# Kernel tuning notes

Measured on AMD Instinct MI355X. Metric: run time of the kernel, lower is better.

The kernel has to match this reference:

```python
import jax, jax.numpy as jnp
import numpy as np

ANGSTROM_TO_METER = 1e-10
COULOMB_CONSTANT = 8987551792.3
ELECTRON_CHARGE = 1.602176634e-19
EV_TO_JOULE = 1.602176634e-19
COUL_DAMPING_BETA = 18.7
R0_METER = 2.2 * ANGSTROM_TO_METER
EWALD_P = 0.3275911
EWALD_A = (0.254829592, -0.284496736, 1.421413741, -1.453152027, 1.061405429)
EWALD_F = 2.0

N_ATOMS = 200000
N_EDGES = 8000000
N_GRAPHS = 256


def setup_inputs() -> dict:
    key = jax.random.key(0)
    k1, k2, k3, k4, k5 = jax.random.split(key, 5)
    dij = jax.random.normal(k1, (N_EDGES, 3), dtype=jnp.float32)  # Angstrom
    pred_charge = jax.random.normal(k2, (N_ATOMS,), dtype=jnp.float32)  # e
    g_ewald = jnp.full((1,), 3.0e9, dtype=jnp.float32)  # 1/m (~0.3 1/A)
    row = jax.random.randint(k3, (N_EDGES,), 0, N_ATOMS)
    col = jax.random.randint(k4, (N_EDGES,), 0, N_ATOMS)
    batch = jnp.sort(jax.random.randint(k5, (N_ATOMS,), 0, N_GRAPHS))
    return {"dij": dij, "pred_charge": pred_charge, "g_ewald": g_ewald,
            "row": row, "col": col, "batch": batch}


def reference(dij, pred_charge, g_ewald, row, col, batch):
    n_atoms = pred_charge.shape[0]
    dij_m = dij * ANGSTROM_TO_METER                      # [E,3] meters
    rij = jnp.sqrt(jnp.sum(dij_m * dij_m, axis=-1))      # [E]
    q = pred_charge * ELECTRON_CHARGE                    # Coulombs
    prefactor = COULOMB_CONSTANT * q[row] * q[col] / rij
    # exponential short-range damping below r0
    damp = jnp.where(rij < R0_METER,
                     jnp.exp(-COUL_DAMPING_BETA * (R0_METER - rij) / R0_METER),
                     jnp.ones_like(rij))
    ecoul = 0.5 * prefactor * damp
    fcoul = prefactor * damp / rij
    # Ewald real-space correction via Abramowitz-Stegun erfc polynomial
    grij = g_ewald[0] * rij
    expm2 = jnp.exp(-grij * grij)
    t = 1.0 / (1.0 + EWALD_P * grij)
    a0, a1, a2, a3, a4 = EWALD_A
    erfc = t * (a0 + t * (a1 + t * (a2 + t * (a3 + t * a4)))) * expm2
    ecoul = ecoul + prefactor * (erfc - 1.0)
    fcoul = fcoul + prefactor * (erfc + EWALD_F * grij * expm2 - 1.0) / rij
    # per-edge force vector, converted J/m -> eV/A
    fij = dij_m * (fcoul / rij)[:, None]                 # [E,3]
    fij_ev = fij * ANGSTROM_TO_METER / EV_TO_JOULE
    ecoul_ev = ecoul / EV_TO_JOULE
    # scatter edge->atom (by row), then atom->molecule (by batch)
    e_atom = jax.ops.segment_sum(ecoul_ev, row, num_segments=n_atoms)
    coul_energy = jax.ops.segment_sum(e_atom, batch, num_segments=N_GRAPHS)
    force_row = jax.ops.segment_sum(fij_ev, row, num_segments=n_atoms)
    force_col = jax.ops.segment_sum(fij_ev, col, num_segments=n_atoms)
    coul_force = force_row - force_col
    return coul_energy, coul_force
```

## Files before the change

kernel.cpp:

```cpp
#include <hip/hip_runtime.h>
#include <hip/hip_fp16.h>

#define N_GRAPHS_C 256
#define CHUNK_LOG 12
#define CHUNK (1 << CHUNK_LOG)
#define MAXB 64
#define NSLICE 12
#define NSLICE_FB 10
#define TPA 256
#define TPBB 512
#define SD 64
#define FP_SCALE 1024.0f
#define FP_INV   (1.0f / 1024.0f)

__device__ __forceinline__ void edge_math(
    float dx, float dy, float dz, float qr, float qc, float gA,
    float& fx, float& fy, float& fz, float& ecoul)
{
    const float KEV = (float)(8987551792.3 * 1.602176634e-9);
    float r2 = dx * dx + dy * dy + dz * dz;
    float inv_r = rsqrtf(r2);
    float rA = r2 * inv_r;

    float pref = KEV * qr * qc * inv_r;

    float damp = 1.0f;
    if (rA < 2.2f)
        damp = __expf(-18.7f * (2.2f - rA) * (1.0f / 2.2f));

    float grij = gA * rA;
    float expm2 = __expf(-grij * grij);
    float t = 1.0f / (1.0f + 0.3275911f * grij);
    float erfc = t * (0.254829592f +
                 t * (-0.284496736f +
                 t * (1.421413741f +
                 t * (-1.453152027f +
                 t * 1.061405429f)))) * expm2;

    ecoul = pref * (0.5f * damp + (erfc - 1.0f));
    float S = damp + erfc + 2.0f * grij * expm2 - 1.0f;
    float fs = pref * S * (inv_r * inv_r);
    fx = dx * fs; fy = dy * fs; fz = dz * fs;
}

__device__ __forceinline__ uint2 pack_rec(float fx, float fy, float fz, unsigned lid)
{
    uint2 u;
    u.x = __builtin_bit_cast(unsigned, __floats2half2_rn(fx, fy));
    u.y = (__builtin_bit_cast(unsigned, __floats2half2_rn(fz, 0.0f)) & 0xFFFFu) |
          (lid << 16);
    return u;
}

__device__ __forceinline__ void acc_rec(int* acc, unsigned w0, unsigned w1)
{
    float2 xy = __half22float2(__builtin_bit_cast(__half2, w0));
    float fz = __half2float(__builtin_bit_cast(__half2, w1).x);
    unsigned idx = w1 >> 16;
    atomicAdd(&acc[idx],             __float2int_rn(xy.x * FP_SCALE));
    atomicAdd(&acc[CHUNK + idx],     __float2int_rn(xy.y * FP_SCALE));
    atomicAdd(&acc[2 * CHUNK + idx], __float2int_rn(fz   * FP_SCALE));
}

__global__ __launch_bounds__(256) void prep_qg(
    const float* __restrict__ q, const int* __restrict__ batch,
    float2* __restrict__ qg, float* __restrict__ ovf, int n_atoms)
{
    int i = blockIdx.x * 256 + threadIdx.x;
    if (i < n_atoms) {
        qg[i] = make_float2(q[i], __int_as_float(batch[i]));
        ovf[3 * i + 0] = 0.f;
        ovf[3 * i + 1] = 0.f;
        ovf[3 * i + 2] = 0.f;
    }
}

__global__ __launch_bounds__(TPA) void passA(
    const float* __restrict__ dij, const float2* __restrict__ qg,
    const float* __restrict__ g_ewald,
    const int* __restrict__ row, const int* __restrict__ col,
    uint2* __restrict__ records, int cap,
    unsigned* __restrict__ cnt_table,
    float* __restrict__ e_part,
    float* __restrict__ ovf,
    int n_edges, int nb, int tile_g)
{
    __shared__ uint2    stage[MAXB][SD];
    __shared__ unsigned scnt[MAXB];
    __shared__ unsigned cnt[MAXB];
    __shared__ float    e_graph[4 * N_GRAPHS_C];

    int tid  = threadIdx.x;
    int wid  = tid >> 6;
    int lane = tid & 63;
    if (tid < MAXB) { scnt[tid] = 0u; cnt[tid] = 0u; }
    for (int i = tid; i < 4 * N_GRAPHS_C; i += TPA) e_graph[i] = 0.f;
    __syncthreads();

    float* e_my = &e_graph[wid * N_GRAPHS_C];

    int n4 = n_edges >> 2;
    int gbase = blockIdx.x * tile_g;
    int g1 = min(gbase + tile_g, n4);
    int nph = tile_g / TPA;

    const int4* row4 = (const int4*)row;
    const int4* col4 = (const int4*)col;
    const float4* dij4 = (const float4*)dij;

    const float gA = g_ewald[0] * 1e-10f;
    size_t blk_base = (size_t)blockIdx.x * nb * cap;

    int4 r_cur = make_int4(0, 0, 0, 0), c_cur = make_int4(0, 0, 0, 0);
    float2 vr_cur[4], vc_cur[4];
    {
        int g = gbase + tid;
        if (g < g1) { r_cur = row4[g]; c_cur = col4[g]; }
        vr_cur[0] = qg[r_cur.x]; vc_cur[0] = qg[c_cur.x];
        vr_cur[1] = qg[r_cur.y]; vc_cur[1] = qg[c_cur.y];
        vr_cur[2] = qg[r_cur.z]; vc_cur[2] = qg[c_cur.z];
        vr_cur[3] = qg[r_cur.w]; vc_cur[3] = qg[c_cur.w];
    }

    for (int p = 0; p < nph; ++p) {
        int g = gbase + p * TPA + tid;

        int4 r_nxt = make_int4(0, 0, 0, 0), c_nxt = make_int4(0, 0, 0, 0);
        if (p + 1 < nph && g + TPA < g1) {
            r_nxt = row4[g + TPA]; c_nxt = col4[g + TPA];
        }

        if (g < g1) {
            float4 d0 = dij4[3 * g + 0];
            float4 d1 = dij4[3 * g + 1];
            float4 d2 = dij4[3 * g + 2];
            float ex[4] = {d0.x, d0.w, d1.z, d2.y};
            float ey[4] = {d0.y, d1.x, d1.w, d2.z};
            float ez[4] = {d0.z, d1.y, d2.x, d2.w};
            int rr[4] = {r_cur.x, r_cur.y, r_cur.z, r_cur.w};
            int cc[4] = {c_cur.x, c_cur.y, c_cur.z, c_cur.w};

            #pragma unroll
            for (int j = 0; j < 4; ++j) {
                int r = rr[j], c = cc[j];
                float fx, fy, fz, ec;
                edge_math(ex[j], ey[j], ez[j], vr_cur[j].x, vc_cur[j].x, gA,
                          fx, fy, fz, ec);

                atomicAdd(&e_my[__float_as_int(vr_cur[j].y)], ec);

                int br = r >> CHUNK_LOG, bc = c >> CHUNK_LOG;
                unsigned pr = atomicAdd(&scnt[br], 1u);
                unsigned pc = atomicAdd(&scnt[bc], 1u);
                if (pr < SD)
                    stage[br][pr] = pack_rec(fx, fy, fz, (unsigned)(r & (CHUNK - 1)));
                else {
                    atomicAdd(&ovf[3 * r + 0], fx);
                    atomicAdd(&ovf[3 * r + 1], fy);
                    atomicAdd(&ovf[3 * r + 2], fz);
                }
                if (pc < SD)
                    stage[bc][pc] = pack_rec(-fx, -fy, -fz, (unsigned)(c & (CHUNK - 1)));
                else {
                    atomicAdd(&ovf[3 * c + 0], -fx);
                    atomicAdd(&ovf[3 * c + 1], -fy);
                    atomicAdd(&ovf[3 * c + 2], -fz);
                }
            }
        }

        float2 vr_n[4], vc_n[4];
        vr_n[0] = qg[r_nxt.x]; vc_n[0] = qg[c_nxt.x];
        vr_n[1] = qg[r_nxt.y]; vc_n[1] = qg[c_nxt.y];
        vr_n[2] = qg[r_nxt.z]; vc_n[2] = qg[c_nxt.z];
        vr_n[3] = qg[r_nxt.w]; vc_n[3] = qg[c_nxt.w];

        __syncthreads();

        for (int b = wid; b < nb; b += TPA / 64) {
            unsigned m = min(scnt[b], (unsigned)SD);
            unsigned base = 0;
            if (lane == 0) base = atomicAdd(&cnt[b], m);
            base = (unsigned)__shfl((int)base, 0, 64);
            for (unsigned i = lane; i < m; i += 64) {
                uint2 rv = stage[b][i];
                unsigned slot = base + i;
                if (slot < (unsigned)cap) {
                    records[blk_base + (size_t)b * cap + slot] = rv;
                } else {
                    float2 xy = __half22float2(__builtin_bit_cast(__half2, rv.x));
                    float fzv = __half2float(__builtin_bit_cast(__half2, rv.y).x);
                    int atom = (b << CHUNK_LOG) + (int)(rv.y >> 16);
                    atomicAdd(&ovf[3 * atom + 0], xy.x);
                    atomicAdd(&ovf[3 * atom + 1], xy.y);
                    atomicAdd(&ovf[3 * atom + 2], fzv);
                }
            }
            if (lane == 0) scnt[b] = 0u;
        }
        __syncthreads();

        r_cur = r_nxt; c_cur = c_nxt;
        #pragma unroll
        for (int j = 0; j < 4; ++j) { vr_cur[j] = vr_n[j]; vc_cur[j] = vc_n[j]; }
    }

    if (tid < nb) cnt_table[(size_t)blockIdx.x * nb + tid] = min(cnt[tid], (unsigned)cap);
    for (int g2 = tid; g2 < N_GRAPHS_C; g2 += TPA)
        e_part[(size_t)blockIdx.x * N_GRAPHS_C + g2] =
            e_graph[g2] + e_graph[N_GRAPHS_C + g2] +
            e_graph[2 * N_GRAPHS_C + g2] + e_graph[3 * N_GRAPHS_C + g2];
}

__global__ __launch_bounds__(TPBB) void passB(
    const uint2* __restrict__ records, int cap,
    const unsigned* __restrict__ cnt_table,
    int* __restrict__ partial, int nblkA, int nb, int nslice)
{
    __shared__ int acc[3 * CHUNK];

    int b = blockIdx.x / nslice;
    int s = blockIdx.x % nslice;
    int k0 = (int)((long long)s * nblkA / nslice);
    int k1 = (int)((long long)(s + 1) * nblkA / nslice);

    for (int i = threadIdx.x; i < 3 * CHUNK; i += TPBB) acc[i] = 0;
    __syncthreads();

    int wid  = threadIdx.x >> 6;
    int lane = threadIdx.x & 63;

    for (int k = k0 + wid; k < k1; k += TPBB / 64) {
        unsigned n = cnt_table[(size_t)k * nb + b];
        const uint2* rec = records + ((size_t)k * nb + b) * cap;
        const uint4* rec4 = (const uint4*)rec;
        unsigned nh = n >> 1;
        for (unsigned i = lane; i < nh; i += 64) {
            uint4 v = rec4[i];
            acc_rec(acc, v.x, v.y);
            acc_rec(acc, v.z, v.w);
        }
        if ((n & 1u) && lane == 0) {
            uint2 t = rec[n - 1];
            acc_rec(acc, t.x, t.y);
        }
    }
    __syncthreads();

    int* dst = partial + (size_t)blockIdx.x * 3 * CHUNK;
    for (int i = threadIdx.x; i < 3 * CHUNK; i += TPBB) dst[i] = acc[i];
}

__global__ __launch_bounds__(256) void fin_force(
    const int* __restrict__ partial, const float* __restrict__ ovf,
    const float* __restrict__ e_part,
    float* __restrict__ force, float* __restrict__ energy,
    int n_atoms, int nslice, int nblkA, int nfblk)
{
    if ((int)blockIdx.x >= nfblk) {
        int g = (blockIdx.x - nfblk) * 4 + (threadIdx.x >> 6);
        int lane = threadIdx.x & 63;
        float s = 0.f;
        for (int k = lane; k < nblkA; k += 64)
            s += e_part[(size_t)k * N_GRAPHS_C + g];
        for (int off = 32; off > 0; off >>= 1) s += __shfl_down(s, off, 64);
        if (lane == 0) energy[g] = s;
        return;
    }
    int a = blockIdx.x * 256 + threadIdx.x;
    if (a >= n_atoms) return;
    int b = a >> CHUNK_LOG, l = a & (CHUNK - 1);
    long long sx = 0, sy = 0, sz = 0;
    const int* p = partial + (size_t)b * nslice * 3 * CHUNK + l;
    for (int s = 0; s < nslice; ++s) {
        const int* ps = p + (size_t)s * 3 * CHUNK;
        sx += ps[0]; sy += ps[CHUNK]; sz += ps[2 * CHUNK];
    }
    force[3 * a + 0] = ovf[3 * a + 0] + (float)sx * FP_INV;
    force[3 * a + 1] = ovf[3 * a + 1] + (float)sy * FP_INV;
    force[3 * a + 2] = ovf[3 * a + 2] + (float)sz * FP_INV;
}

__global__ __launch_bounds__(1024) void chunk_kernel(
    const float* __restrict__ dij, const float* __restrict__ q,
    const float* __restrict__ g_ewald,
    const int* __restrict__ row, const int* __restrict__ col,
    float* __restrict__ partial, int n_edges, int n_chunks, int n_slices)
{
    __shared__ float acc[CHUNK * 4];
    int c = blockIdx.x % n_chunks;
    int p = blockIdx.x / n_chunks;
    int cbase = c << CHUNK_LOG;
    for (int i = threadIdx.x; i < CHUNK * 4; i += 1024) acc[i] = 0.f;
    __syncthreads();
    const float gA = g_ewald[0] * 1e-10f;
    int n4 = (n_edges + 3) >> 2;
    int g0 = (int)((long long)p * n4 / n_slices);
    int g1 = (int)((long long)(p + 1) * n4 / n_slices);
    const int4* row4 = (const int4*)row;
    const int4* col4 = (const int4*)col;
    for (int g = g0 + threadIdx.x; g < g1; g += 1024) {
        int4 r4 = row4[g];
        int4 c4 = col4[g];
        int rr[4] = {r4.x, r4.y, r4.z, r4.w};
        int cc[4] = {c4.x, c4.y, c4.z, c4.w};
        #pragma unroll
        for (int j = 0; j < 4; ++j) {
            int e = 4 * g + j;
            if (e >= n_edges) break;
            int rl = rr[j] - cbase;
            int cl = cc[j] - cbase;
            bool hr = (unsigned)rl < (unsigned)CHUNK;
            bool hc = (unsigned)cl < (unsigned)CHUNK;
            if (!(hr || hc)) continue;
            float fx, fy, fz, ec;
            edge_math(dij[3 * e], dij[3 * e + 1], dij[3 * e + 2],
                      q[rr[j]], q[cc[j]], gA, fx, fy, fz, ec);
            if (hr) {
                atomicAdd(&acc[4 * rl + 0], fx);
                atomicAdd(&acc[4 * rl + 1], fy);
                atomicAdd(&acc[4 * rl + 2], fz);
                atomicAdd(&acc[4 * rl + 3], ec);
            }
            if (hc) {
                atomicAdd(&acc[4 * cl + 0], -fx);
                atomicAdd(&acc[4 * cl + 1], -fy);
                atomicAdd(&acc[4 * cl + 2], -fz);
            }
        }
    }
    __syncthreads();
    float4* dst = (float4*)partial + (size_t)(c * n_slices + p) * CHUNK;
    const float4* src = (const float4*)acc;
    for (int i = threadIdx.x; i < CHUNK; i += 1024) dst[i] = src[i];
}

__global__ __launch_bounds__(256) void finalize_kernel(
    const float* __restrict__ partial, const int* __restrict__ batch,
    float* __restrict__ energy, float* __restrict__ force,
    int n_atoms, int n_slices)
{
    int i = blockIdx.x * blockDim.x + threadIdx.x;
    float fx = 0.f, fy = 0.f, fz = 0.f, en = 0.f;
    if (i < n_atoms) {
        int c = i >> CHUNK_LOG;
        int l = i & (CHUNK - 1);
        const float4* base = (const float4*)partial + (size_t)c * n_slices * CHUNK + l;
        for (int p = 0; p < n_slices; ++p) {
            float4 v = base[(size_t)p * CHUNK];
            fx += v.x; fy += v.y; fz += v.z; en += v.w;
        }
        force[3 * i + 0] = fx;
        force[3 * i + 1] = fy;
        force[3 * i + 2] = fz;
    }
    int ic = i < n_atoms ? i : (n_atoms - 1);
    int b = batch[ic];
    float v = (i < n_atoms) ? en : 0.0f;
    int b0 = __shfl(b, 0, 64);
    unsigned long long m = __ballot(b == b0);
    if (m == ~0ull) {
        for (int off = 32; off > 0; off >>= 1)
            v += __shfl_down(v, off, 64);
        if ((threadIdx.x & 63) == 0) atomicAdd(&energy[b0], v);
    } else {
        atomicAdd(&energy[b], v);
    }
}

extern "C" void kernel_launch(void* const* d_in, const int* in_sizes, int n_in,
                              void* d_out, int out_size, void* d_ws, size_t ws_size,
                              hipStream_t stream) {
    const float* dij     = (const float*)d_in[0];
    const float* q       = (const float*)d_in[1];
    const float* g_ewald = (const float*)d_in[2];
    const int*   row     = (const int*)d_in[3];
    const int*   col     = (const int*)d_in[4];
    const int*   batch   = (const int*)d_in[5];

    int n_edges = in_sizes[0] / 3;
    int n_atoms = in_sizes[1];

    float* energy = (float*)d_out;
    float* force  = (float*)d_out + N_GRAPHS_C;

    int nb = (n_atoms + CHUNK - 1) >> CHUNK_LOG;
    int n4 = n_edges >> 2;

    size_t sz_partial = (size_t)nb * NSLICE * 3 * CHUNK * sizeof(int);
    size_t sz_ovf     = (size_t)3 * n_atoms * sizeof(float);
    size_t sz_qg      = (size_t)n_atoms * sizeof(float2);

    const int  tile_sel[2]   = {1024, 2048};
    const int  mincap_sel[2] = {224, 416};
    const int  capmax_sel[2] = {256, 512};

    int tile_g = 0, cap = 0, nblkA = 0;
    size_t sz_epart = 0, sz_cnt = 0;
    for (int t = 0; t < 2 && tile_g == 0; ++t) {
        int nba = (n4 + tile_sel[t] - 1) / tile_sel[t];
        size_t se = (size_t)nba * N_GRAPHS_C * sizeof(float);
        size_t sc = (size_t)nba * nb * sizeof(unsigned);
        size_t fixed = ((sz_partial + 255) & ~(size_t)255) +
                       ((se         + 255) & ~(size_t)255) +
                       ((sc         + 255) & ~(size_t)255) +
                       ((sz_ovf     + 255) & ~(size_t)255) +
                       ((sz_qg      + 255) & ~(size_t)255) + 512;
        if ((long long)ws_size > (long long)fixed) {
            long long c = ((long long)ws_size - (long long)fixed) /
                          ((long long)nba * nb * 8);
            c = (c / 32) * 32;
            if (c > capmax_sel[t]) c = capmax_sel[t];
            if (c >= mincap_sel[t]) {
                tile_g = tile_sel[t]; cap = (int)c; nblkA = nba;
                sz_epart = se; sz_cnt = sc;
            }
        }
    }

    bool fast = (nb <= MAXB) && ((n_edges & 3) == 0) && (tile_g > 0) &&
                ((tile_g % TPA) == 0);

    if (fast) {
        char* ws = (char*)d_ws;
        size_t off = 0;
        uint2*    records  = (uint2*)(ws + off);
        off += (size_t)nblkA * nb * cap * 8;   off = (off + 255) & ~(size_t)255;
        int*      partial  = (int*)(ws + off);
        off += sz_partial;                     off = (off + 255) & ~(size_t)255;
        float*    e_part   = (float*)(ws + off);
        off += sz_epart;                       off = (off + 255) & ~(size_t)255;
        unsigned* cnt_tab  = (unsigned*)(ws + off);
        off += sz_cnt;                         off = (off + 255) & ~(size_t)255;
        float*    ovf      = (float*)(ws + off);
        off += sz_ovf;                         off = (off + 255) & ~(size_t)255;
        float2*   qg       = (float2*)(ws + off);

        prep_qg<<<(n_atoms + 255) / 256, 256, 0, stream>>>(q, batch, qg, ovf, n_atoms);

        passA<<<nblkA, TPA, 0, stream>>>(
            dij, qg, g_ewald, row, col,
            records, cap, cnt_tab, e_part, ovf, n_edges, nb, tile_g);

        passB<<<nb * NSLICE, TPBB, 0, stream>>>(
            records, cap, cnt_tab, partial, nblkA, nb, NSLICE);

        int nfblk = (n_atoms + 255) / 256;
        fin_force<<<nfblk + N_GRAPHS_C / 4, 256, 0, stream>>>(
            partial, ovf, e_part, force, energy, n_atoms, NSLICE, nblkA, nfblk);
    } else {
        size_t need_chunk = (size_t)nb * NSLICE_FB * CHUNK * 4 * sizeof(float);
        if (ws_size >= need_chunk) {
            hipMemsetAsync(d_out, 0, N_GRAPHS_C * sizeof(float), stream);
            chunk_kernel<<<nb * NSLICE_FB, 1024, 0, stream>>>(
                dij, q, g_ewald, row, col, (float*)d_ws, n_edges, nb, NSLICE_FB);
            finalize_kernel<<<(n_atoms + 255) / 256, 256, 0, stream>>>(
                (const float*)d_ws, batch, energy, force, n_atoms, NSLICE_FB);
        }
    }
}
```

Measured before the change: 360.2 us.

## Batch four record lists per wave in passB, pad stage array, raise slice count

In passB each wave now loads the counts and records of four bucket lists at once, issuing four independent vector loads per iteration before accumulating. This raises memory-level parallelism and hides load latency better than walking one list at a time. The slice count also goes from 12 to 16, giving more passB blocks and more partial buffers for the finalize step to reduce. The passA shared staging array is padded by one element to cut LDS bank conflicts. The cost is extra redundant, clamped loads when list lengths differ, and more registers per thread.

```diff
diff --git a/kernel.cpp b/kernel.cpp
--- a/kernel.cpp
+++ b/kernel.cpp
@@ -5,7 +5,7 @@
 #define CHUNK_LOG 12
 #define CHUNK (1 << CHUNK_LOG)
 #define MAXB 64
-#define NSLICE 12
+#define NSLICE 16
 #define NSLICE_FB 10
 #define TPA 256
 #define TPBB 512
@@ -85,7 +85,7 @@
     float* __restrict__ ovf,
     int n_edges, int nb, int tile_g)
 {
-    __shared__ uint2    stage[MAXB][SD];
+    __shared__ uint2    stage[MAXB][SD + 1];
     __shared__ unsigned scnt[MAXB];
     __shared__ unsigned cnt[MAXB];
     __shared__ float    e_graph[4 * N_GRAPHS_C];
@@ -229,20 +229,44 @@
 
     int wid  = threadIdx.x >> 6;
     int lane = threadIdx.x & 63;
-
-    for (int k = k0 + wid; k < k1; k += TPBB / 64) {
-        unsigned n = cnt_table[(size_t)k * nb + b];
-        const uint2* rec = records + ((size_t)k * nb + b) * cap;
-        const uint4* rec4 = (const uint4*)rec;
-        unsigned nh = n >> 1;
-        for (unsigned i = lane; i < nh; i += 64) {
-            uint4 v = rec4[i];
-            acc_rec(acc, v.x, v.y);
-            acc_rec(acc, v.z, v.w);
-        }
-        if ((n & 1u) && lane == 0) {
-            uint2 t = rec[n - 1];
-            acc_rec(acc, t.x, t.y);
+    const int W = TPBB / 64;
+
+    for (int kb = k0 + wid; kb < k1; kb += 4 * W) {
+        int ka = kb, kB = kb + W, kc = kb + 2 * W, kd = kb + 3 * W;
+        bool e1 = kB < k1, e2 = kc < k1, e3 = kd < k1;
+
+        unsigned n0 = cnt_table[(size_t)ka * nb + b];
+        unsigned n1 = e1 ? cnt_table[(size_t)kB * nb + b] : 0u;
+        unsigned n2 = e2 ? cnt_table[(size_t)kc * nb + b] : 0u;
+        unsigned n3 = e3 ? cnt_table[(size_t)kd * nb + b] : 0u;
+
+        const uint2* r0 = records + ((size_t)ka * nb + b) * cap;
+        const uint2* r1 = e1 ? records + ((size_t)kB * nb + b) * cap : r0;
+        const uint2* r2 = e2 ? records + ((size_t)kc * nb + b) * cap : r0;
+        const uint2* r3 = e3 ? records + ((size_t)kd * nb + b) * cap : r0;
+        const uint4* q0 = (const uint4*)r0;
+        const uint4* q1 = (const uint4*)r1;
+        const uint4* q2 = (const uint4*)r2;
+        const uint4* q3 = (const uint4*)r3;
+
+        unsigned h0 = n0 >> 1, h1 = n1 >> 1, h2 = n2 >> 1, h3 = n3 >> 1;
+        unsigned hm = max(max(h0, h1), max(h2, h3));
+
+        for (unsigned i = lane; i < hm; i += 64) {
+            uint4 v0 = q0[h0 ? min(i, h0 - 1u) : 0u];
+            uint4 v1 = q1[h1 ? min(i, h1 - 1u) : 0u];
+            uint4 v2 = q2[h2 ? min(i, h2 - 1u) : 0u];
+            uint4 v3 = q3[h3 ? min(i, h3 - 1u) : 0u];
+            if (i < h0) { acc_rec(acc, v0.x, v0.y); acc_rec(acc, v0.z, v0.w); }
+            if (i < h1) { acc_rec(acc, v1.x, v1.y); acc_rec(acc, v1.z, v1.w); }
+            if (i < h2) { acc_rec(acc, v2.x, v2.y); acc_rec(acc, v2.z, v2.w); }
+            if (i < h3) { acc_rec(acc, v3.x, v3.y); acc_rec(acc, v3.z, v3.w); }
+        }
+        if (lane == 0) {
+            if (n0 & 1u) { uint2 t = r0[n0 - 1]; acc_rec(acc, t.x, t.y); }
+            if (n1 & 1u) { uint2 t = r1[n1 - 1]; acc_rec(acc, t.x, t.y); }
+            if (n2 & 1u) { uint2 t = r2[n2 - 1]; acc_rec(acc, t.x, t.y); }
+            if (n3 & 1u) { uint2 t = r3[n3 - 1]; acc_rec(acc, t.x, t.y); }
         }
     }
     __syncthreads();
```

After: 352.3 us. 2.2% less time.
